# Kernel tuning notes

Hardware: AMD Instinct MI355X
Metric: run time of the kernel (lower is better)

## Reference

```python
import jax, jax.numpy as jnp
import numpy as np

QMIN, QMAX = -128, 127


def setup_inputs() -> dict:
    key = jax.random.key(0)
    kx, kw, kb = jax.random.split(key, 3)
    B, S, IN, OUT = 4, 2048, 4096, 4096
    x = jax.random.normal(kx, (B, S, IN), dtype=jnp.float32)
    # int8-valued weight stored as int32 for portability
    weight_int = jax.random.randint(kw, (OUT, IN), QMIN, QMAX + 1, dtype=jnp.int32)
    bias = jax.random.normal(kb, (OUT,), dtype=jnp.float32) * 0.02
    # plausible frozen qparams: x~N(0,1) -> range ~[-4,4]; weight range ~[-3,3] pre-quant
    scale_a = jnp.asarray(8.0 / 255.0, dtype=jnp.float32)
    zp_a = jnp.asarray(0, dtype=jnp.int32)
    weight_scale = jnp.asarray(6.0 / 255.0, dtype=jnp.float32)
    weight_zero_point = jnp.asarray(0, dtype=jnp.int32)
    return {
        "x": x,
        "weight_int": weight_int,
        "bias": bias,
        "scale_a": scale_a,
        "zp_a": zp_a,
        "weight_scale": weight_scale,
        "weight_zero_point": weight_zero_point,
    }


def reference(x, weight_int, bias, scale_a, zp_a, weight_scale, weight_zero_point):
    # fake-quantize activations: round(x/scale)+zp, clamp to int8 range
    zp_a_f = zp_a.astype(jnp.float32)
    x_int8 = jnp.clip(jnp.round(x / scale_a) + zp_a_f, QMIN, QMAX)
    x_cent = x_int8 - zp_a_f                                   # [B,S,IN]
    w_cent = weight_int.astype(jnp.float32) - weight_zero_point.astype(jnp.float32)  # [OUT,IN]
    y = jnp.einsum("bsi,oi->bso", x_cent, w_cent)              # dequant-space GEMM
    y = y * (scale_a * weight_scale)
    y = y + bias
    return y
```

## Files before the change

### kernel.cpp

```cpp
#include <hip/hip_runtime.h>
#include <stdint.h>

typedef int v4i  __attribute__((ext_vector_type(4)));
typedef int v16i __attribute__((ext_vector_type(16)));

__global__ void quant_fused_kernel(const float* __restrict__ x,
                                   const int* __restrict__ w,
                                   int8_t* __restrict__ xq,
                                   int8_t* __restrict__ wq,
                                   int* __restrict__ sum_x,
                                   int* __restrict__ sum_w,
                                   const float* __restrict__ p_scale,
                                   const int* __restrict__ p_zp,
                                   int M, int K) {
    const int t = threadIdx.x;
    const int nchunk = K >> 10;
    int lsum = 0;
    if (blockIdx.x < M) {
        const int row = blockIdx.x;
        const float s = p_scale[0];
        const float zpf = (float)p_zp[0];
        const float* xr = x + (size_t)row * K;
        int8_t* qr = xq + (size_t)row * K;
        for (int i = 0; i < nchunk; ++i) {
            const int idx = (i << 10) + (t << 2);
            const float4 v = *reinterpret_cast<const float4*>(xr + idx);
            const float f0 = fminf(fmaxf(rintf(v.x / s) + zpf, -128.f), 127.f);
            const float f1 = fminf(fmaxf(rintf(v.y / s) + zpf, -128.f), 127.f);
            const float f2 = fminf(fmaxf(rintf(v.z / s) + zpf, -128.f), 127.f);
            const float f3 = fminf(fmaxf(rintf(v.w / s) + zpf, -128.f), 127.f);
            const int i0 = (int)f0, i1 = (int)f1, i2 = (int)f2, i3 = (int)f3;
            lsum += i0 + i1 + i2 + i3;
            const unsigned pk = (unsigned)(i0 & 255) | ((unsigned)(i1 & 255) << 8) |
                                ((unsigned)(i2 & 255) << 16) | ((unsigned)(i3 & 255) << 24);
            *reinterpret_cast<unsigned*>(qr + idx) = pk;
        }
    } else {
        const int row = blockIdx.x - M;
        const int* wr_ = w + (size_t)row * K;
        int8_t* qr = wq + (size_t)row * K;
        for (int i = 0; i < nchunk; ++i) {
            const int idx = (i << 10) + (t << 2);
            const int4 v = *reinterpret_cast<const int4*>(wr_ + idx);
            lsum += v.x + v.y + v.z + v.w;
            const unsigned pk = (unsigned)(v.x & 255) | ((unsigned)(v.y & 255) << 8) |
                                ((unsigned)(v.z & 255) << 16) | ((unsigned)(v.w & 255) << 24);
            *reinterpret_cast<unsigned*>(qr + idx) = pk;
        }
    }
    __shared__ int wsum[4];
    #pragma unroll
    for (int off = 32; off > 0; off >>= 1) lsum += __shfl_down(lsum, off);
    if ((t & 63) == 0) wsum[t >> 6] = lsum;
    __syncthreads();
    if (t == 0) {
        const int tot = wsum[0] + wsum[1] + wsum[2] + wsum[3];
        if (blockIdx.x < M) sum_x[blockIdx.x] = tot;
        else                sum_w[blockIdx.x - M] = tot;
    }
}

#define BM 256
#define BN 256
#define BKB 64
#define NSLOT 4

__device__ __forceinline__ void gload_lds16(const void* g, void* l) {
    __builtin_amdgcn_global_load_lds(
        (const __attribute__((address_space(1))) unsigned int*)g,
        (__attribute__((address_space(3))) unsigned int*)l, 16, 0, 0);
}

#define MFMA_I8 __builtin_amdgcn_mfma_i32_32x32x32_i8

__global__ __launch_bounds__(256, 1)
void gemm_i8_kernel(const int8_t* __restrict__ xq,
                    const int8_t* __restrict__ wq,
                    const int* __restrict__ sum_x,
                    const int* __restrict__ sum_w,
                    const float* __restrict__ bias,
                    float* __restrict__ out,
                    const float* __restrict__ p_sa,
                    const int* __restrict__ p_zpa,
                    const float* __restrict__ p_sw,
                    const int* __restrict__ p_wzp,
                    int M, int N, int K) {
    __shared__ v4i ldsA[NSLOT][1024];
    __shared__ v4i ldsB[NSLOT][1024];

    const int tid = threadIdx.x;
    const int lane = tid & 63;
    const int wid = tid >> 6;
    const int wr = wid >> 1;
    const int wc = wid & 1;

    const int nwgy = M / BM;
    const int nwgx = N / BN;
    const int spx = nwgy >> 3;
    const int bid = blockIdx.x;
    const int xcd = bid & 7;
    const int loc = bid >> 3;
    const int m0 = (xcd * spx + loc / nwgx) * BM;
    const int n0 = (loc % nwgx) * BN;

    const int srow = tid >> 2;
    const int schunk = (tid & 3) ^ (((srow >> 1) ^ (srow >> 3)) & 3);
    const int8_t* aS = xq + (size_t)(m0 + srow) * K + schunk * 16;
    const int8_t* bS = wq + (size_t)(n0 + srow) * K + schunk * 16;
    const size_t qtr = (size_t)64 * K;
    const int dbase = wid * 64;

    const int sel = ((lane >> 1) ^ (lane >> 3)) & 3;
    const int hi = lane >> 5;
    const int c0 = hi ^ sel;
    const int c1 = (2 + hi) ^ sel;
    int arow[4], brow[4];
    #pragma unroll
    for (int i = 0; i < 4; ++i) {
        arow[i] = (wr * 128 + i * 32 + (lane & 31)) * 4;
        brow[i] = (wc * 128 + i * 32 + (lane & 31)) * 4;
    }

    v16i acc[4][4] = {};
    const int NT = K / BKB;

#define STAGE(SLOT, T_) do {                                                  \
        const int8_t* pa_ = aS + (size_t)(T_) * BKB;                          \
        const int8_t* pb_ = bS + (size_t)(T_) * BKB;                          \
        _Pragma("unroll")                                                     \
        for (int k_ = 0; k_ < 4; ++k_) {                                      \
            gload_lds16(pa_ + k_ * qtr, &ldsA[SLOT][k_ * 256 + dbase]);       \
            gload_lds16(pb_ + k_ * qtr, &ldsB[SLOT][k_ * 256 + dbase]);       \
        }                                                                     \
    } while (0)

    STAGE(0, 0);
    STAGE(1, 1);
    asm volatile("s_waitcnt vmcnt(8)" ::: "memory");
    __builtin_amdgcn_sched_barrier(0);
    __builtin_amdgcn_s_barrier();

    for (int t = 0; t < NT; ++t) {
        const v4i* LA = ldsA[t & 3];
        const v4i* LB = ldsB[t & 3];
        v4i a[4][2], b[4][2];
        #pragma unroll
        for (int i = 0; i < 4; ++i) {
            a[i][0] = LA[arow[i] + c0];
            a[i][1] = LA[arow[i] + c1];
        }
        #pragma unroll
        for (int i = 0; i < 4; ++i) {
            b[i][0] = LB[brow[i] + c0];
            b[i][1] = LB[brow[i] + c1];
        }
        if (t + 2 < NT) STAGE((t + 2) & 3, t + 2);
        __builtin_amdgcn_s_setprio(1);
        #pragma unroll
        for (int ks = 0; ks < 2; ++ks)
            #pragma unroll
            for (int rf = 0; rf < 4; ++rf)
                #pragma unroll
                for (int cf = 0; cf < 4; ++cf)
                    acc[rf][cf] = MFMA_I8(a[rf][ks], b[cf][ks], acc[rf][cf], 0, 0, 0);
        __builtin_amdgcn_s_setprio(0);
        if (t + 2 < NT) {
            asm volatile("s_waitcnt vmcnt(8)" ::: "memory");
        } else if (t + 1 < NT) {
            asm volatile("s_waitcnt vmcnt(0)" ::: "memory");
        }
        __builtin_amdgcn_sched_barrier(0);
        __builtin_amdgcn_s_barrier();
    }
#undef STAGE

    const float stot = p_sa[0] * p_sw[0];
    const int zpa = p_zpa[0];
    const int wzp = p_wzp[0];
    const int kzz = K * zpa * wzp;
    const int coll = lane & 31;
    const int rhi = (lane >> 5) * 4;

    #pragma unroll
    for (int cf = 0; cf < 4; ++cf) {
        const int cg = n0 + wc * 128 + cf * 32 + coll;
        const int sw = sum_w[cg];
        const float bb = bias[cg];
        #pragma unroll
        for (int rf = 0; rf < 4; ++rf) {
            const int rbase = m0 + wr * 128 + rf * 32 + rhi;
            #pragma unroll
            for (int r = 0; r < 16; ++r) {
                const int rowg = rbase + (r & 3) + 8 * (r >> 2);
                const int iv = acc[rf][cf][r] - wzp * sum_x[rowg] - zpa * sw + kzz;
                out[(size_t)rowg * N + cg] = (float)iv * stot + bb;
            }
        }
    }
}

extern "C" void kernel_launch(void* const* d_in, const int* in_sizes, int n_in,
                              void* d_out, int out_size, void* d_ws, size_t ws_size,
                              hipStream_t stream) {
    const float* x     = (const float*)d_in[0];
    const int*   w     = (const int*)d_in[1];
    const float* bias  = (const float*)d_in[2];
    const float* p_sa  = (const float*)d_in[3];
    const int*   p_zpa = (const int*)d_in[4];
    const float* p_sw  = (const float*)d_in[5];
    const int*   p_wzp = (const int*)d_in[6];

    const int N = in_sizes[2];
    const int K = in_sizes[1] / N;
    const int M = in_sizes[0] / K;

    int8_t* xq = (int8_t*)d_ws;
    int8_t* wq = xq + (size_t)M * K;
    int* sum_x = (int*)(wq + (size_t)N * K);
    int* sum_w = sum_x + M;

    quant_fused_kernel<<<M + N, 256, 0, stream>>>(x, w, xq, wq, sum_x, sum_w,
                                                  p_sa, p_zpa, M, K);

    const int nwg = (M / BM) * (N / BN);
    gemm_i8_kernel<<<nwg, 256, 0, stream>>>(xq, wq, sum_x, sum_w, bias,
                                            (float*)d_out, p_sa, p_zpa, p_sw, p_wzp,
                                            M, N, K);
}
```

Baseline: 229.0 us.

## Make LDS staging wave-private to drop workgroup barriers in int8 GEMM

Each wave now loads its own 128-row slices of A and B into a private LDS region, so the main loop no longer needs an s_barrier between waves. The shared four-slot ring with a two-tile prefetch becomes a per-wave double buffer with a one-tile prefetch, and each iteration waits with vmcnt(0). This removes cross-wave synchronisation stalls. In exchange, every A and B row is fetched twice (by two waves), doubling global/L2 traffic into LDS, and the shallower prefetch gives less room to hide load latency.

```diff
diff --git a/kernel.cpp b/kernel.cpp
--- a/kernel.cpp
+++ b/kernel.cpp
@@ -63,7 +63,6 @@
 #define BM 256
 #define BN 256
 #define BKB 64
-#define NSLOT 4
 
 __device__ __forceinline__ void gload_lds16(const void* g, void* l) {
     __builtin_amdgcn_global_load_lds(
@@ -85,8 +84,8 @@
                     const float* __restrict__ p_sw,
                     const int* __restrict__ p_wzp,
                     int M, int N, int K) {
-    __shared__ v4i ldsA[NSLOT][1024];
-    __shared__ v4i ldsB[NSLOT][1024];
+    __shared__ v4i ldsAp[4][2][512];
+    __shared__ v4i ldsBp[4][2][512];
 
     const int tid = threadIdx.x;
     const int lane = tid & 63;
@@ -103,58 +102,55 @@
     const int m0 = (xcd * spx + loc / nwgx) * BM;
     const int n0 = (loc % nwgx) * BN;
 
-    const int srow = tid >> 2;
-    const int schunk = (tid & 3) ^ (((srow >> 1) ^ (srow >> 3)) & 3);
-    const int8_t* aS = xq + (size_t)(m0 + srow) * K + schunk * 16;
-    const int8_t* bS = wq + (size_t)(n0 + srow) * K + schunk * 16;
-    const size_t qtr = (size_t)64 * K;
-    const int dbase = wid * 64;
+    const int8_t* aW = xq + (size_t)(m0 + wr * 128) * K;
+    const int8_t* bW = wq + (size_t)(n0 + wc * 128) * K;
+    int off[8];
+    #pragma unroll
+    for (int j = 0; j < 8; ++j) {
+        const int r = j * 16 + (lane >> 2);
+        const int sc = (lane & 3) ^ (((r >> 1) ^ (r >> 3)) & 3);
+        off[j] = r * K + sc * 16;
+    }
 
     const int sel = ((lane >> 1) ^ (lane >> 3)) & 3;
     const int hi = lane >> 5;
     const int c0 = hi ^ sel;
     const int c1 = (2 + hi) ^ sel;
-    int arow[4], brow[4];
-    #pragma unroll
-    for (int i = 0; i < 4; ++i) {
-        arow[i] = (wr * 128 + i * 32 + (lane & 31)) * 4;
-        brow[i] = (wc * 128 + i * 32 + (lane & 31)) * 4;
-    }
+    int frow[4];
+    #pragma unroll
+    for (int i = 0; i < 4; ++i) frow[i] = (i * 32 + (lane & 31)) * 4;
 
     v16i acc[4][4] = {};
     const int NT = K / BKB;
 
 #define STAGE(SLOT, T_) do {                                                  \
-        const int8_t* pa_ = aS + (size_t)(T_) * BKB;                          \
-        const int8_t* pb_ = bS + (size_t)(T_) * BKB;                          \
+        const int kof_ = (T_) * BKB;                                          \
         _Pragma("unroll")                                                     \
-        for (int k_ = 0; k_ < 4; ++k_) {                                      \
-            gload_lds16(pa_ + k_ * qtr, &ldsA[SLOT][k_ * 256 + dbase]);       \
-            gload_lds16(pb_ + k_ * qtr, &ldsB[SLOT][k_ * 256 + dbase]);       \
+        for (int j = 0; j < 8; ++j) {                                         \
+            gload_lds16(aW + kof_ + off[j], &ldsAp[wid][SLOT][j * 64]);       \
+            gload_lds16(bW + kof_ + off[j], &ldsBp[wid][SLOT][j * 64]);       \
         }                                                                     \
     } while (0)
 
     STAGE(0, 0);
-    STAGE(1, 1);
-    asm volatile("s_waitcnt vmcnt(8)" ::: "memory");
+    asm volatile("s_waitcnt vmcnt(0)" ::: "memory");
     __builtin_amdgcn_sched_barrier(0);
-    __builtin_amdgcn_s_barrier();
 
     for (int t = 0; t < NT; ++t) {
-        const v4i* LA = ldsA[t & 3];
-        const v4i* LB = ldsB[t & 3];
+        if (t + 1 < NT) STAGE((t + 1) & 1, t + 1);
+        const v4i* LA = ldsAp[wid][t & 1];
+        const v4i* LB = ldsBp[wid][t & 1];
         v4i a[4][2], b[4][2];
         #pragma unroll
         for (int i = 0; i < 4; ++i) {
-            a[i][0] = LA[arow[i] + c0];
-            a[i][1] = LA[arow[i] + c1];
+            a[i][0] = LA[frow[i] + c0];
+            a[i][1] = LA[frow[i] + c1];
         }
         #pragma unroll
         for (int i = 0; i < 4; ++i) {
-            b[i][0] = LB[brow[i] + c0];
-            b[i][1] = LB[brow[i] + c1];
-        }
-        if (t + 2 < NT) STAGE((t + 2) & 3, t + 2);
+            b[i][0] = LB[frow[i] + c0];
+            b[i][1] = LB[frow[i] + c1];
+        }
         __builtin_amdgcn_s_setprio(1);
         #pragma unroll
         for (int ks = 0; ks < 2; ++ks)
@@ -164,13 +160,10 @@
                 for (int cf = 0; cf < 4; ++cf)
                     acc[rf][cf] = MFMA_I8(a[rf][ks], b[cf][ks], acc[rf][cf], 0, 0, 0);
         __builtin_amdgcn_s_setprio(0);
-        if (t + 2 < NT) {
-            asm volatile("s_waitcnt vmcnt(8)" ::: "memory");
-        } else if (t + 1 < NT) {
+        if (t + 1 < NT) {
             asm volatile("s_waitcnt vmcnt(0)" ::: "memory");
-        }
-        __builtin_amdgcn_sched_barrier(0);
-        __builtin_amdgcn_s_barrier();
+            __builtin_amdgcn_sched_barrier(0);
+        }
     }
 #undef STAGE
 
```

After: 254.4 us. +11.1%, slower.
